# Performance work log

Hardware: AMD Instinct MI355X
Metric: run time of the kernel (lower is better)

## Reference

```python
import jax, jax.numpy as jnp
import numpy as np

N_NODES = 100000
N_EDGES = 1600000
DIM = 128
HEADS = 8
PHC = DIM // HEADS  # per-head channels = 16


def setup_inputs() -> dict:
    key = jax.random.key(0)
    k1, k2, k3, k4, k5 = jax.random.split(key, 5)
    nodes = jax.random.normal(k1, (N_NODES, DIM), dtype=jnp.float32)
    senders = jax.random.randint(k2, (N_EDGES,), 0, N_NODES, dtype=jnp.int32)
    receivers = jax.random.randint(k3, (N_EDGES,), 0, N_NODES, dtype=jnp.int32)
    # VarianceScaling(fan_avg, uniform) ~ limit = sqrt(3/fan_avg)
    lim_w = np.sqrt(3.0 / DIM)
    W = jax.random.uniform(k4, (DIM, DIM), minval=-lim_w, maxval=lim_w, dtype=jnp.float32)
    b = jnp.zeros((DIM,), dtype=jnp.float32)
    lim_a = np.sqrt(3.0 * 2.0 / (2 * PHC + 1))
    attn_w = jax.random.uniform(k5, (2 * PHC, 1), minval=-lim_a, maxval=lim_a, dtype=jnp.float32)
    attn_b = jnp.zeros((1,), dtype=jnp.float32)
    return {"nodes": nodes, "senders": senders, "receivers": receivers,
            "W": W, "b": b, "attn_w": attn_w, "attn_b": attn_b}


def reference(nodes, senders, receivers, W, b, attn_w, attn_b):
    n = nodes.shape[0]
    # linear transform + split heads: [N, H, PHC]
    nt = (nodes @ W + b).reshape(n, HEADS, PHC)
    sent = nt[senders]      # [E, H, PHC] gather
    recv = nt[receivers]    # [E, H, PHC] gather
    # attention logits: Linear(1) over leaky_relu(concat(q,k)) -> [E, H, 1]
    qk = jax.nn.leaky_relu(jnp.concatenate([sent, recv], axis=-1), negative_slope=0.2)
    logits = qk @ attn_w + attn_b  # [E, H, 1]
    # segment softmax over edges grouped by receiver node
    seg_max = jax.ops.segment_max(logits, receivers, num_segments=n)  # [N, H, 1]
    exp = jnp.exp(logits - seg_max[receivers])
    denom = jax.ops.segment_sum(exp, receivers, num_segments=n)  # [N, H, 1]
    alpha = exp / denom[receivers]
    # weighted scatter-sum of sender features
    out = jax.ops.segment_sum(sent * alpha, receivers, num_segments=n)  # [N, H, PHC]
    return out.reshape(n, -1)  # concat=True -> [N, DIM]
```

## Files before the change

### kernel.cpp

```cpp
#include <hip/hip_runtime.h>

#define DIM 128
#define HEADS 8
#define PHC 16

#define BSHIFT 6
#define BNODES 64
#define CAP 1408
#define NBMAX 1600

typedef __bf16 bf16x4 __attribute__((ext_vector_type(4)));
typedef __bf16 bf16x8 __attribute__((ext_vector_type(8)));
typedef float  f32x4  __attribute__((ext_vector_type(4)));

__device__ inline unsigned short f2bf(float x) {
  unsigned int u = __float_as_uint(x);
  unsigned int r = (u + 0x7FFF + ((u >> 16) & 1)) >> 16;
  return (unsigned short)r;
}

__global__ __launch_bounds__(256) void k_prepw(
    const float* __restrict__ W, __bf16* __restrict__ Wh,
    __bf16* __restrict__ Wl, int* __restrict__ gCursor, int NB) {
  const int tuple = blockIdx.x * 256 + threadIdx.x;
  if (tuple < NB) gCursor[tuple] = 0;
  const int ln = tuple & 15;
  const int lg = (tuple >> 4) & 3;
  const int cg = (tuple >> 6) & 7;
  const int kt = tuple >> 9;
  const int col = (cg << 4) + ln;
  bf16x8 h, l;
#pragma unroll
  for (int e = 0; e < 8; ++e) {
    int k = (kt << 5) + ((e >> 2) << 4) + (lg << 2) + (e & 3);
    float wv = W[k * DIM + col];
    __bf16 hh = (__bf16)wv;
    h[e] = hh;
    l[e] = (__bf16)(wv - (float)hh);
  }
  *(bf16x8*)(Wh + tuple * 8) = h;
  *(bf16x8*)(Wl + tuple * 8) = l;
}

#define GROWS 64

__global__ __launch_bounds__(256, 3) void k_gemm_scatter(
    const float* __restrict__ A, const __bf16* __restrict__ Wh,
    const __bf16* __restrict__ Wl, const float* __restrict__ bias,
    const float* __restrict__ attn_w, unsigned int* __restrict__ nt_bf,
    float* __restrict__ s_exp, const int* __restrict__ send,
    const int* __restrict__ recv, int* __restrict__ gCursor,
    unsigned int* __restrict__ pairs, int E, int NB, int nScat, int n) {
  __shared__ __align__(16) float smemF[GROWS * DIM];

  if (blockIdx.x < nScat) {
    int* cnt = (int*)smemF;
    int* cur = cnt + NBMAX;
    const int t = threadIdx.x;
    for (int i = t; i < NB; i += 256) cnt[i] = 0;
    __syncthreads();
    const int e0 = blockIdx.x * 8192;
    const int e1 = min(e0 + 8192, E);
    for (int i = e0 + t; i < e1; i += 256)
      atomicAdd(&cnt[recv[i] >> BSHIFT], 1);
    __syncthreads();
    for (int i = t; i < NB; i += 256) {
      int c = cnt[i];
      cur[i] = i * CAP + (c ? atomicAdd(&gCursor[i], c) : 0);
    }
    __syncthreads();
    for (int i = e0 + t; i < e1; i += 256) {
      int r = recv[i];
      int b = r >> BSHIFT;
      int p = atomicAdd(&cur[b], 1);
      if (p - b * CAP < CAP)
        pairs[p] = (unsigned int)send[i] | ((unsigned int)(r & (BNODES - 1)) << 17);
    }
    return;
  }

  __bf16* Ah = (__bf16*)smemF;
  __bf16* Al = Ah + GROWS * DIM;
  const int t    = threadIdx.x;
  const int row0 = (blockIdx.x - nScat) * GROWS;
  const int lane = t & 63;
  const int w    = t >> 6;
  const int lg   = lane >> 4;
  const int ln   = lane & 15;

  float4 av[8];
  {
    const float4* A4 = (const float4*)(A + (size_t)row0 * DIM);
    const int lim = min(GROWS, n - row0) * (DIM / 4);
#pragma unroll
    for (int j = 0; j < 8; ++j) {
      int i = t + j * 256;
      av[j] = (i < lim) ? A4[i] : make_float4(0.f, 0.f, 0.f, 0.f);
    }
  }

#pragma unroll
  for (int j = 0; j < 8; ++j) {
    int i = t + j * 256;
    int r = i >> 5, c4 = i & 31;
    int ktc = c4 >> 3, lgc = c4 & 3, ehi = (c4 >> 2) & 1;
    int unit = (r << 4) + (((ktc << 2) + lgc) ^ (r & 15));
    int ei = (unit << 3) + (ehi << 2);
    float x0 = av[j].x, x1 = av[j].y, x2 = av[j].z, x3 = av[j].w;
    __bf16 h0 = (__bf16)x0, h1 = (__bf16)x1, h2 = (__bf16)x2, h3 = (__bf16)x3;
    bf16x4 hv = {h0, h1, h2, h3};
    bf16x4 lv = {(__bf16)(x0 - (float)h0), (__bf16)(x1 - (float)h1),
                 (__bf16)(x2 - (float)h2), (__bf16)(x3 - (float)h3)};
    *(bf16x4*)(Ah + ei) = hv;
    *(bf16x4*)(Al + ei) = lv;
  }

  f32x4 acc[4][2];
  {
    const float b0 = bias[(w << 5) + ln];
    const float b1 = bias[(w << 5) + 16 + ln];
#pragma unroll
    for (int rt = 0; rt < 4; ++rt) {
      acc[rt][0] = (f32x4){b0, b0, b0, b0};
      acc[rt][1] = (f32x4){b1, b1, b1, b1};
    }
  }
  __syncthreads();

  const int cg0 = w << 1;
#pragma unroll
  for (int kt = 0; kt < 4; ++kt) {
    bf16x8 Bh0, Bl0, Bh1, Bl1;
    {
      int i0 = ((((kt << 3) + cg0) << 2) + lg) * 16 + ln;
      int i1 = ((((kt << 3) + cg0 + 1) << 2) + lg) * 16 + ln;
      Bh0 = *(const bf16x8*)(Wh + (i0 << 3));
      Bl0 = *(const bf16x8*)(Wl + (i0 << 3));
      Bh1 = *(const bf16x8*)(Wh + (i1 << 3));
      Bl1 = *(const bf16x8*)(Wl + (i1 << 3));
    }
    bf16x8 ah[4], al[4];
#pragma unroll
    for (int rt = 0; rt < 4; ++rt) {
      int m = (rt << 4) + ln;
      int u = (m << 4) + (((kt << 2) + lg) ^ (m & 15));
      ah[rt] = *(const bf16x8*)(Ah + (u << 3));
      al[rt] = *(const bf16x8*)(Al + (u << 3));
    }
#pragma unroll
    for (int rt = 0; rt < 4; ++rt) {
      acc[rt][0] = __builtin_amdgcn_mfma_f32_16x16x32_bf16(ah[rt], Bh0, acc[rt][0], 0, 0, 0);
      acc[rt][0] = __builtin_amdgcn_mfma_f32_16x16x32_bf16(ah[rt], Bl0, acc[rt][0], 0, 0, 0);
      acc[rt][0] = __builtin_amdgcn_mfma_f32_16x16x32_bf16(al[rt], Bh0, acc[rt][0], 0, 0, 0);
      acc[rt][1] = __builtin_amdgcn_mfma_f32_16x16x32_bf16(ah[rt], Bh1, acc[rt][1], 0, 0, 0);
      acc[rt][1] = __builtin_amdgcn_mfma_f32_16x16x32_bf16(ah[rt], Bl1, acc[rt][1], 0, 0, 0);
      acc[rt][1] = __builtin_amdgcn_mfma_f32_16x16x32_bf16(al[rt], Bh1, acc[rt][1], 0, 0, 0);
    }
  }

  __syncthreads();

#pragma unroll
  for (int rt = 0; rt < 4; ++rt)
#pragma unroll
    for (int ct = 0; ct < 2; ++ct) {
      int colx = ((w << 5) + (ct << 4) + ln) ^ ((lg & 1) << 4);
#pragma unroll
      for (int r = 0; r < 4; ++r) {
        int rowl = (rt << 4) + (lg << 2) + r;
        smemF[(rowl << 7) + colx] = acc[rt][ct][r];
      }
    }

  {
    const float aw = attn_w[ln];
#pragma unroll
    for (int rt = 0; rt < 4; ++rt)
#pragma unroll
      for (int ct = 0; ct < 2; ++ct) {
        const int head = (w << 1) + ct;
#pragma unroll
        for (int r = 0; r < 4; ++r) {
          float v = acc[rt][ct][r];
          float p = (v > 0.f ? v : 0.2f * v) * aw;
          p += __shfl_xor(p, 1);
          p += __shfl_xor(p, 2);
          p += __shfl_xor(p, 4);
          p += __shfl_xor(p, 8);
          if (ln == 0) {
            int row = row0 + (rt << 4) + (lg << 2) + r;
            if (row < n) s_exp[row * HEADS + head] = __expf(p);
          }
        }
      }
  }
  __syncthreads();

  {
    const int nrow = min(GROWS, n - row0);
#pragma unroll
    for (int j = 0; j < 8; ++j) {
      int i = t + j * 256;
      int r = i >> 5, c4 = i & 31;
      if (r < nrow) {
        int c4s = c4 ^ (((r >> 2) & 1) << 2);
        f32x4 v = *(const f32x4*)(smemF + (r << 7) + (c4s << 2));
        unsigned int lo = (unsigned int)f2bf(v[0]) | ((unsigned int)f2bf(v[1]) << 16);
        unsigned int hi = (unsigned int)f2bf(v[2]) | ((unsigned int)f2bf(v[3]) << 16);
        ((uint2*)nt_bf)[(size_t)(row0 + r) * 32 + c4] = make_uint2(lo, hi);
      }
    }
  }
}

__device__ inline void acc8(float wgt, uint4 qv, float4& a0, float4& a1) {
  a0.x = fmaf(wgt, __uint_as_float(qv.x << 16), a0.x);
  a0.y = fmaf(wgt, __uint_as_float(qv.x & 0xFFFF0000u), a0.y);
  a0.z = fmaf(wgt, __uint_as_float(qv.y << 16), a0.z);
  a0.w = fmaf(wgt, __uint_as_float(qv.y & 0xFFFF0000u), a0.w);
  a1.x = fmaf(wgt, __uint_as_float(qv.z << 16), a1.x);
  a1.y = fmaf(wgt, __uint_as_float(qv.z & 0xFFFF0000u), a1.y);
  a1.z = fmaf(wgt, __uint_as_float(qv.w << 16), a1.z);
  a1.w = fmaf(wgt, __uint_as_float(qv.w & 0xFFFF0000u), a1.w);
}

__global__ __launch_bounds__(256) void k_aggbuild(
    const unsigned int* __restrict__ pairs, const int* __restrict__ gCursor,
    const unsigned int* __restrict__ nt_bf, const float* __restrict__ s_exp,
    float* __restrict__ out, int n) {
  __shared__ unsigned int buf[CAP];
  __shared__ int csr_l[CAP];
  __shared__ int hist[BNODES], offl[BNODES], curl[BNODES];
  const int b = blockIdx.x >> 1;
  const int c = blockIdx.x & 1;
  const int t = threadIdx.x;
  const int base = b * CAP;
  const int bsize = min(gCursor[b], CAP);

  for (int i = t; i < bsize; i += 256) buf[i] = pairs[base + i];
  if (t < BNODES) hist[t] = 0;
  __syncthreads();
  for (int i = t; i < bsize; i += 256)
    atomicAdd(&hist[(buf[i] >> 17) & (BNODES - 1)], 1);
  __syncthreads();
  if (t < 64) {
    int v = hist[t];
    int x = v;
#pragma unroll
    for (int off = 1; off < 64; off <<= 1) {
      int y = __shfl_up(x, off);
      if (t >= off) x += y;
    }
    offl[t] = x - v;
    curl[t] = x - v;
  }
  __syncthreads();
  for (int i = t; i < bsize; i += 256) {
    unsigned int v = buf[i];
    int p = atomicAdd(&curl[(v >> 17) & (BNODES - 1)], 1);
    csr_l[p] = (int)(v & 0x1FFFF);
  }
  __syncthreads();

  const int wv   = t >> 6;
  const int lane = t & 63;
  const int e8   = lane >> 3;
  const int l8   = lane & 7;
  const int head = (c << 2) + (l8 >> 1);
  const int uoff = (c << 3) + l8;
  const uint4* nt4 = (const uint4*)nt_bf;

#pragma unroll 1
  for (int pi = 0; pi < 2; ++pi) {
    const int nl = (wv << 4) + (pi << 3) + e8;
    const int node = (b << BSHIFT) + nl;
    const int deg = hist[nl];
    const int eoff = offl[nl];
    float4 a0 = make_float4(0.f, 0.f, 0.f, 0.f);
    float4 a1 = make_float4(0.f, 0.f, 0.f, 0.f);
    float den = 0.f;
    for (int j = 0; j < deg; j += 4) {
      bool ok1 = (j + 1) < deg, ok2 = (j + 2) < deg, ok3 = (j + 3) < deg;
      int s0 = csr_l[eoff + j];
      int s1 = csr_l[ok1 ? (eoff + j + 1) : eoff];
      int s2 = csr_l[ok2 ? (eoff + j + 2) : eoff];
      int s3 = csr_l[ok3 ? (eoff + j + 3) : eoff];
      float w0 = s_exp[s0 * HEADS + head];
      float w1 = ok1 ? s_exp[s1 * HEADS + head] : 0.f;
      float w2 = ok2 ? s_exp[s2 * HEADS + head] : 0.f;
      float w3 = ok3 ? s_exp[s3 * HEADS + head] : 0.f;
      uint4 q0 = nt4[(size_t)s0 * 16 + uoff];
      uint4 q1 = nt4[(size_t)s1 * 16 + uoff];
      uint4 q2 = nt4[(size_t)s2 * 16 + uoff];
      uint4 q3 = nt4[(size_t)s3 * 16 + uoff];
      den += (w0 + w1) + (w2 + w3);
      acc8(w0, q0, a0, a1);
      acc8(w1, q1, a0, a1);
      acc8(w2, q2, a0, a1);
      acc8(w3, q3, a0, a1);
    }
    if (node < n) {
      const float inv = (deg > 0) ? 1.0f / den : 0.f;
      float4* op = (float4*)out + (size_t)node * 32 + (c << 4) + (l8 << 1);
      op[0] = make_float4(a0.x * inv, a0.y * inv, a0.z * inv, a0.w * inv);
      op[1] = make_float4(a1.x * inv, a1.y * inv, a1.z * inv, a1.w * inv);
    }
  }
}

extern "C" void kernel_launch(void* const* d_in, const int* in_sizes, int n_in,
                              void* d_out, int out_size, void* d_ws, size_t ws_size,
                              hipStream_t stream) {
  const float* nodes   = (const float*)d_in[0];
  const int*   senders = (const int*)d_in[1];
  const int*   recvs   = (const int*)d_in[2];
  const float* W       = (const float*)d_in[3];
  const float* bias    = (const float*)d_in[4];
  const float* attn_w  = (const float*)d_in[5];

  const int n = in_sizes[0] / DIM;
  const int E = in_sizes[1];
  const int NB = (n + BNODES - 1) >> BSHIFT;

  char* w = (char*)d_ws;
  auto align256 = [](size_t x) { return (x + 255) & ~(size_t)255; };
  size_t off = 0;
  unsigned int* nt_bf = (unsigned int*)(w + off); off += align256((size_t)n * DIM * 2);
  float* s_exp   = (float*)(w + off); off += align256((size_t)n * HEADS * 4);
  unsigned int* pairs = (unsigned int*)(w + off); off += align256((size_t)NB * CAP * 4);
  int* gCursor   = (int*)(w + off);   off += align256((size_t)NB * 4);
  __bf16* Wh     = (__bf16*)(w + off); off += align256((size_t)2048 * 8 * 2);
  __bf16* Wl     = (__bf16*)(w + off); off += align256((size_t)2048 * 8 * 2);
  (void)ws_size;

  k_prepw<<<8, 256, 0, stream>>>(W, Wh, Wl, gCursor, NB);
  const int nScat = (E + 8191) / 8192;
  const int ngemm = (n + GROWS - 1) / GROWS;
  k_gemm_scatter<<<nScat + ngemm, 256, 0, stream>>>(
      nodes, Wh, Wl, bias, attn_w, nt_bf, s_exp,
      senders, recvs, gCursor, pairs, E, NB, nScat, n);
  k_aggbuild<<<NB * 2, 256, 0, stream>>>(pairs, gCursor, nt_bf, s_exp,
                                         (float*)d_out, n);
}
```

Baseline: 252.1 us.

## Store node features and exp logits head-major; split aggregation per head

Transformed node features (bf16) and the per-node exp weights are now written in head-major layout: features as [head][node][16 channels] and weights as [head][node]. The aggregation kernel launches one block per (node bucket, head), so each block's gathers touch a single contiguous per-head plane, which should improve cache locality for random sender gathers. The cost is that every block rebuilds the bucket's local CSR (loading the pairs, histogram, scan, fill), so that work is now done eight times per bucket instead of twice. Nontemporal loads and stores are added for the pair buffer and the output.

```diff
diff --git a/kernel.cpp b/kernel.cpp
--- a/kernel.cpp
+++ b/kernel.cpp
@@ -47,8 +47,8 @@
 __global__ __launch_bounds__(256, 3) void k_gemm_scatter(
     const float* __restrict__ A, const __bf16* __restrict__ Wh,
     const __bf16* __restrict__ Wl, const float* __restrict__ bias,
-    const float* __restrict__ attn_w, unsigned int* __restrict__ nt_bf,
-    float* __restrict__ s_exp, const int* __restrict__ send,
+    const float* __restrict__ attn_w, unsigned int* __restrict__ nt_t,
+    float* __restrict__ s_exp_t, const int* __restrict__ send,
     const int* __restrict__ recv, int* __restrict__ gCursor,
     unsigned int* __restrict__ pairs, int E, int NB, int nScat, int n) {
   __shared__ __align__(16) float smemF[GROWS * DIM];
@@ -189,7 +189,7 @@
           p += __shfl_xor(p, 8);
           if (ln == 0) {
             int row = row0 + (rt << 4) + (lg << 2) + r;
-            if (row < n) s_exp[row * HEADS + head] = __expf(p);
+            if (row < n) s_exp_t[(size_t)head * n + row] = __expf(p);
           }
         }
       }
@@ -198,46 +198,37 @@
 
   {
     const int nrow = min(GROWS, n - row0);
-#pragma unroll
-    for (int j = 0; j < 8; ++j) {
-      int i = t + j * 256;
-      int r = i >> 5, c4 = i & 31;
-      if (r < nrow) {
+    const int r = t >> 2;
+    const int q = t & 3;
+    if (r < nrow) {
+#pragma unroll
+      for (int j = 0; j < 8; ++j) {
+        int c4 = (j << 2) + q;
         int c4s = c4 ^ (((r >> 2) & 1) << 2);
         f32x4 v = *(const f32x4*)(smemF + (r << 7) + (c4s << 2));
         unsigned int lo = (unsigned int)f2bf(v[0]) | ((unsigned int)f2bf(v[1]) << 16);
         unsigned int hi = (unsigned int)f2bf(v[2]) | ((unsigned int)f2bf(v[3]) << 16);
-        ((uint2*)nt_bf)[(size_t)(row0 + r) * 32 + c4] = make_uint2(lo, hi);
+        ((uint2*)nt_t)[((size_t)j * n + row0 + r) * 4 + q] = make_uint2(lo, hi);
       }
     }
   }
-}
-
-__device__ inline void acc8(float wgt, uint4 qv, float4& a0, float4& a1) {
-  a0.x = fmaf(wgt, __uint_as_float(qv.x << 16), a0.x);
-  a0.y = fmaf(wgt, __uint_as_float(qv.x & 0xFFFF0000u), a0.y);
-  a0.z = fmaf(wgt, __uint_as_float(qv.y << 16), a0.z);
-  a0.w = fmaf(wgt, __uint_as_float(qv.y & 0xFFFF0000u), a0.w);
-  a1.x = fmaf(wgt, __uint_as_float(qv.z << 16), a1.x);
-  a1.y = fmaf(wgt, __uint_as_float(qv.z & 0xFFFF0000u), a1.y);
-  a1.z = fmaf(wgt, __uint_as_float(qv.w << 16), a1.z);
-  a1.w = fmaf(wgt, __uint_as_float(qv.w & 0xFFFF0000u), a1.w);
 }
 
 __global__ __launch_bounds__(256) void k_aggbuild(
     const unsigned int* __restrict__ pairs, const int* __restrict__ gCursor,
-    const unsigned int* __restrict__ nt_bf, const float* __restrict__ s_exp,
+    const unsigned int* __restrict__ nt_t, const float* __restrict__ s_exp_t,
     float* __restrict__ out, int n) {
   __shared__ unsigned int buf[CAP];
   __shared__ int csr_l[CAP];
   __shared__ int hist[BNODES], offl[BNODES], curl[BNODES];
-  const int b = blockIdx.x >> 1;
-  const int c = blockIdx.x & 1;
+  const int b = blockIdx.x >> 3;
+  const int h = blockIdx.x & 7;
   const int t = threadIdx.x;
   const int base = b * CAP;
   const int bsize = min(gCursor[b], CAP);
 
-  for (int i = t; i < bsize; i += 256) buf[i] = pairs[base + i];
+  for (int i = t; i < bsize; i += 256)
+    buf[i] = __builtin_nontemporal_load(&pairs[base + i]);
   if (t < BNODES) hist[t] = 0;
   __syncthreads();
   for (int i = t; i < bsize; i += 256)
@@ -262,49 +253,54 @@
   }
   __syncthreads();
 
-  const int wv   = t >> 6;
-  const int lane = t & 63;
-  const int e8   = lane >> 3;
-  const int l8   = lane & 7;
-  const int head = (c << 2) + (l8 >> 1);
-  const int uoff = (c << 3) + l8;
-  const uint4* nt4 = (const uint4*)nt_bf;
-
-#pragma unroll 1
-  for (int pi = 0; pi < 2; ++pi) {
-    const int nl = (wv << 4) + (pi << 3) + e8;
-    const int node = (b << BSHIFT) + nl;
-    const int deg = hist[nl];
-    const int eoff = offl[nl];
-    float4 a0 = make_float4(0.f, 0.f, 0.f, 0.f);
-    float4 a1 = make_float4(0.f, 0.f, 0.f, 0.f);
-    float den = 0.f;
-    for (int j = 0; j < deg; j += 4) {
-      bool ok1 = (j + 1) < deg, ok2 = (j + 2) < deg, ok3 = (j + 3) < deg;
-      int s0 = csr_l[eoff + j];
-      int s1 = csr_l[ok1 ? (eoff + j + 1) : eoff];
-      int s2 = csr_l[ok2 ? (eoff + j + 2) : eoff];
-      int s3 = csr_l[ok3 ? (eoff + j + 3) : eoff];
-      float w0 = s_exp[s0 * HEADS + head];
-      float w1 = ok1 ? s_exp[s1 * HEADS + head] : 0.f;
-      float w2 = ok2 ? s_exp[s2 * HEADS + head] : 0.f;
-      float w3 = ok3 ? s_exp[s3 * HEADS + head] : 0.f;
-      uint4 q0 = nt4[(size_t)s0 * 16 + uoff];
-      uint4 q1 = nt4[(size_t)s1 * 16 + uoff];
-      uint4 q2 = nt4[(size_t)s2 * 16 + uoff];
-      uint4 q3 = nt4[(size_t)s3 * 16 + uoff];
-      den += (w0 + w1) + (w2 + w3);
-      acc8(w0, q0, a0, a1);
-      acc8(w1, q1, a0, a1);
-      acc8(w2, q2, a0, a1);
-      acc8(w3, q3, a0, a1);
-    }
-    if (node < n) {
-      const float inv = (deg > 0) ? 1.0f / den : 0.f;
-      float4* op = (float4*)out + (size_t)node * 32 + (c << 4) + (l8 << 1);
-      op[0] = make_float4(a0.x * inv, a0.y * inv, a0.z * inv, a0.w * inv);
-      op[1] = make_float4(a1.x * inv, a1.y * inv, a1.z * inv, a1.w * inv);
-    }
+  const int nl = t >> 2;
+  const int q  = t & 3;
+  const int node = (b << BSHIFT) + nl;
+  const int deg = hist[nl];
+  const int eoff = offl[nl];
+  const uint2* nt2 = (const uint2*)nt_t;
+  const float* sp = s_exp_t + (size_t)h * n;
+  const size_t pb4 = (size_t)h * n * 4;
+
+  f32x4 a = {0.f, 0.f, 0.f, 0.f};
+  float den = 0.f;
+  for (int j = 0; j < deg; j += 4) {
+    bool ok1 = (j + 1) < deg, ok2 = (j + 2) < deg, ok3 = (j + 3) < deg;
+    int s0 = csr_l[eoff + j];
+    int s1 = csr_l[ok1 ? (eoff + j + 1) : eoff];
+    int s2 = csr_l[ok2 ? (eoff + j + 2) : eoff];
+    int s3 = csr_l[ok3 ? (eoff + j + 3) : eoff];
+    float w0 = sp[s0];
+    float w1 = ok1 ? sp[s1] : 0.f;
+    float w2 = ok2 ? sp[s2] : 0.f;
+    float w3 = ok3 ? sp[s3] : 0.f;
+    uint2 q0 = nt2[pb4 + s0 * 4 + q];
+    uint2 q1 = nt2[pb4 + s1 * 4 + q];
+    uint2 q2 = nt2[pb4 + s2 * 4 + q];
+    uint2 q3 = nt2[pb4 + s3 * 4 + q];
+    den += (w0 + w1) + (w2 + w3);
+    a.x = fmaf(w0, __uint_as_float(q0.x << 16),
+          fmaf(w1, __uint_as_float(q1.x << 16),
+          fmaf(w2, __uint_as_float(q2.x << 16),
+          fmaf(w3, __uint_as_float(q3.x << 16), a.x))));
+    a.y = fmaf(w0, __uint_as_float(q0.x & 0xFFFF0000u),
+          fmaf(w1, __uint_as_float(q1.x & 0xFFFF0000u),
+          fmaf(w2, __uint_as_float(q2.x & 0xFFFF0000u),
+          fmaf(w3, __uint_as_float(q3.x & 0xFFFF0000u), a.y))));
+    a.z = fmaf(w0, __uint_as_float(q0.y << 16),
+          fmaf(w1, __uint_as_float(q1.y << 16),
+          fmaf(w2, __uint_as_float(q2.y << 16),
+          fmaf(w3, __uint_as_float(q3.y << 16), a.z))));
+    a.w = fmaf(w0, __uint_as_float(q0.y & 0xFFFF0000u),
+          fmaf(w1, __uint_as_float(q1.y & 0xFFFF0000u),
+          fmaf(w2, __uint_as_float(q2.y & 0xFFFF0000u),
+          fmaf(w3, __uint_as_float(q3.y & 0xFFFF0000u), a.w))));
+  }
+  if (node < n) {
+    const float inv = (deg > 0) ? 1.0f / den : 0.f;
+    f32x4 o = {a.x * inv, a.y * inv, a.z * inv, a.w * inv};
+    __builtin_nontemporal_store(
+        o, (f32x4*)out + (size_t)node * 32 + (h << 2) + q);
   }
 }
 
@@ -325,8 +321,8 @@
   char* w = (char*)d_ws;
   auto align256 = [](size_t x) { return (x + 255) & ~(size_t)255; };
   size_t off = 0;
-  unsigned int* nt_bf = (unsigned int*)(w + off); off += align256((size_t)n * DIM * 2);
-  float* s_exp   = (float*)(w + off); off += align256((size_t)n * HEADS * 4);
+  unsigned int* nt_t = (unsigned int*)(w + off); off += align256((size_t)n * DIM * 2);
+  float* s_exp_t = (float*)(w + off); off += align256((size_t)n * HEADS * 4);
   unsigned int* pairs = (unsigned int*)(w + off); off += align256((size_t)NB * CAP * 4);
   int* gCursor   = (int*)(w + off);   off += align256((size_t)NB * 4);
   __bf16* Wh     = (__bf16*)(w + off); off += align256((size_t)2048 * 8 * 2);
@@ -337,8 +333,8 @@
   const int nScat = (E + 8191) / 8192;
   const int ngemm = (n + GROWS - 1) / GROWS;
   k_gemm_scatter<<<nScat + ngemm, 256, 0, stream>>>(
-      nodes, Wh, Wl, bias, attn_w, nt_bf, s_exp,
+      nodes, Wh, Wl, bias, attn_w, nt_t, s_exp_t,
       senders, recvs, gCursor, pairs, E, NB, nScat, n);
-  k_aggbuild<<<NB * 2, 256, 0, stream>>>(pairs, gCursor, nt_bf, s_exp,
+  k_aggbuild<<<NB * 8, 256, 0, stream>>>(pairs, gCursor, nt_t, s_exp_t,
                                          (float*)d_out, n);
 }
```

Measured after the change: 294.0 us. 1.17x slower.

## Merge channel-half blocks into one and sort nodes by degree for load balance

Applied to the files above, without the earlier changes.

The aggregation kernel previously launched two blocks per 64-node bucket, each handling half the channels, so the per-bucket CSR build in shared memory ran twice. Now one block handles all 128 channels with 16 lanes per node, and nodes are assigned to wavefront slots in descending-degree order via a rank computed with shuffles, so nodes with similar degree share a wavefront and divergence is reduced. Pair loads also become nontemporal. This halves the block count and the redundant bucket sort, but each block now does more gather work, which may reduce latency hiding.

```diff
diff --git a/kernel.cpp b/kernel.cpp
--- a/kernel.cpp
+++ b/kernel.cpp
@@ -230,14 +230,15 @@
     float* __restrict__ out, int n) {
   __shared__ unsigned int buf[CAP];
   __shared__ int csr_l[CAP];
-  __shared__ int hist[BNODES], offl[BNODES], curl[BNODES];
-  const int b = blockIdx.x >> 1;
-  const int c = blockIdx.x & 1;
+  __shared__ int hist[BNODES], curl[BNODES];
+  __shared__ unsigned int slotmeta[BNODES];
+  const int b = blockIdx.x;
   const int t = threadIdx.x;
   const int base = b * CAP;
   const int bsize = min(gCursor[b], CAP);
 
-  for (int i = t; i < bsize; i += 256) buf[i] = pairs[base + i];
+  for (int i = t; i < bsize; i += 256)
+    buf[i] = __builtin_nontemporal_load(&pairs[base + i]);
   if (t < BNODES) hist[t] = 0;
   __syncthreads();
   for (int i = t; i < bsize; i += 256)
@@ -251,8 +252,15 @@
       int y = __shfl_up(x, off);
       if (t >= off) x += y;
     }
-    offl[t] = x - v;
-    curl[t] = x - v;
+    int e = x - v;
+    curl[t] = e;
+    int rank = 0;
+    for (int j = 0; j < 64; ++j) {
+      int dj = __shfl(v, j);
+      rank += (dj > v) || (dj == v && j < t);
+    }
+    slotmeta[rank] = ((unsigned int)e << 17) | ((unsigned int)v << 6) |
+                     (unsigned int)t;
   }
   __syncthreads();
   for (int i = t; i < bsize; i += 256) {
@@ -264,18 +272,18 @@
 
   const int wv   = t >> 6;
   const int lane = t & 63;
-  const int e8   = lane >> 3;
-  const int l8   = lane & 7;
-  const int head = (c << 2) + (l8 >> 1);
-  const int uoff = (c << 3) + l8;
+  const int q    = lane >> 4;
+  const int l16  = lane & 15;
+  const int head = l16 >> 1;
   const uint4* nt4 = (const uint4*)nt_bf;
 
 #pragma unroll 1
-  for (int pi = 0; pi < 2; ++pi) {
-    const int nl = (wv << 4) + (pi << 3) + e8;
-    const int node = (b << BSHIFT) + nl;
-    const int deg = hist[nl];
-    const int eoff = offl[nl];
+  for (int pi = 0; pi < 4; ++pi) {
+    const int slot = (pi << 4) + (wv << 2) + q;
+    const unsigned int m = slotmeta[slot];
+    const int node = (b << BSHIFT) + (int)(m & 63);
+    const int deg  = (int)((m >> 6) & 0x7FF);
+    const int eoff = (int)(m >> 17);
     float4 a0 = make_float4(0.f, 0.f, 0.f, 0.f);
     float4 a1 = make_float4(0.f, 0.f, 0.f, 0.f);
     float den = 0.f;
@@ -289,10 +297,10 @@
       float w1 = ok1 ? s_exp[s1 * HEADS + head] : 0.f;
       float w2 = ok2 ? s_exp[s2 * HEADS + head] : 0.f;
       float w3 = ok3 ? s_exp[s3 * HEADS + head] : 0.f;
-      uint4 q0 = nt4[(size_t)s0 * 16 + uoff];
-      uint4 q1 = nt4[(size_t)s1 * 16 + uoff];
-      uint4 q2 = nt4[(size_t)s2 * 16 + uoff];
-      uint4 q3 = nt4[(size_t)s3 * 16 + uoff];
+      uint4 q0 = nt4[(size_t)s0 * 16 + l16];
+      uint4 q1 = nt4[(size_t)s1 * 16 + l16];
+      uint4 q2 = nt4[(size_t)s2 * 16 + l16];
+      uint4 q3 = nt4[(size_t)s3 * 16 + l16];
       den += (w0 + w1) + (w2 + w3);
       acc8(w0, q0, a0, a1);
       acc8(w1, q1, a0, a1);
@@ -301,7 +309,7 @@
     }
     if (node < n) {
       const float inv = (deg > 0) ? 1.0f / den : 0.f;
-      float4* op = (float4*)out + (size_t)node * 32 + (c << 4) + (l8 << 1);
+      float4* op = (float4*)out + (size_t)node * 32 + l16 * 2;
       op[0] = make_float4(a0.x * inv, a0.y * inv, a0.z * inv, a0.w * inv);
       op[1] = make_float4(a1.x * inv, a1.y * inv, a1.z * inv, a1.w * inv);
     }
@@ -339,6 +347,6 @@
   k_gemm_scatter<<<nScat + ngemm, 256, 0, stream>>>(
       nodes, Wh, Wl, bias, attn_w, nt_bf, s_exp,
       senders, recvs, gCursor, pairs, E, NB, nScat, n);
-  k_aggbuild<<<NB * 2, 256, 0, stream>>>(pairs, gCursor, nt_bf, s_exp,
-                                         (float*)d_out, n);
-}
+  k_aggbuild<<<NB, 256, 0, stream>>>(pairs, gCursor, nt_bf, s_exp,
+                                     (float*)d_out, n);
+}
```

Result: faster. 245.0 us (-2.8%).
